# Kernel optimization log

Measured on AMD Instinct MI355X. Metric: run time of the kernel, lower is better.

The kernel has to match this reference:

```python
import jax, jax.numpy as jnp
import numpy as np

# CE module constants (from init_kwargs / chosen input shape)
K = 7        # ksize
S1 = 4       # stride_1 (query patches / fold stride)
S2 = 1       # stride_2 (key/value patches)
SCALE = 10.0 # softmax_scale
C_IN = 32    # in_channels
IC = 4       # inter_channels
B, H, W = 2, 128, 128
PAD1 = ((1, 2), (1, 2))  # 'same' padding for k=7, stride=4, H=W=128 (top=1,bot=2)
PAD2 = ((3, 3), (3, 3))  # 'same' padding for k=7, stride=1


def _conv(x, w, b, stride, pad):
    y = jax.lax.conv_general_dilated(x, w, (stride, stride), pad,
                                     dimension_numbers=('NCHW', 'OIHW', 'NCHW'))
    return y + b[None, :, None, None]


def _patches(x, k, stride, pad):
    # returns [B, L, C*k*k] with feature order (C, kh, kw) == torch.nn.Unfold
    p = jax.lax.conv_general_dilated_patches(x, (k, k), (stride, stride), padding=pad)
    bb, f, ho, wo = p.shape
    return p.reshape(bb, f, ho * wo).transpose(0, 2, 1), ho, wo


def _fold_norm(out, ic, k, hh, ww, stride, pad, lh, lw):
    # out: [B, L1, ic*k*k] -> F.fold(..., (hh,ww), k, padding=pad, stride=stride),
    # normalized by overlap count fold(unfold(ones)).
    bb = out.shape[0]
    z = out.reshape(bb, lh, lw, ic, k, k).transpose(0, 3, 1, 2, 4, 5)  # [B,ic,lh,lw,k,k]
    hp, wp = hh + 2 * pad, ww + 2 * pad
    acc = jnp.zeros((bb, ic, hp, wp), out.dtype)
    cnt = jnp.zeros((hp, wp), out.dtype)
    ih = jnp.arange(lh) * stride
    iw = jnp.arange(lw) * stride
    one = jnp.ones((lh, lw), out.dtype)
    for ki in range(k):
        for kj in range(k):
            r = (ih + ki)[:, None]
            c = (iw + kj)[None, :]
            acc = acc.at[:, :, r, c].add(z[:, :, :, :, ki, kj])
            cnt = cnt.at[r, c].add(one)
    acc = acc[:, :, pad:pad + hh, pad:pad + ww]
    cnt = cnt[pad:pad + hh, pad:pad + ww]
    return acc / cnt


def setup_inputs() -> dict:
    key = jax.random.key(0)
    ks = jax.random.split(key, 13)
    f = K * K * IC  # 196
    g = f // 4      # 49
    s = 0.05
    return {
        'b':       jax.random.normal(ks[0], (B, C_IN, H, W), jnp.float32),
        'w_g':     (jax.random.normal(ks[1], (IC, C_IN, 3, 3), jnp.float32) * s),
        'b_g':     jnp.zeros((IC,), jnp.float32),
        'w_theta': (jax.random.normal(ks[2], (IC, C_IN, 1, 1), jnp.float32) * s),
        'b_theta': jnp.zeros((IC,), jnp.float32),
        'w_fc1':   (jax.random.normal(ks[3], (g, f), jnp.float32) * s),
        'b_fc1':   jnp.zeros((g,), jnp.float32),
        'w_fc2':   (jax.random.normal(ks[4], (g, f), jnp.float32) * s),
        'b_fc2':   jnp.zeros((g,), jnp.float32),
        'w_thr':   (jax.random.normal(ks[5], (1, C_IN, K, K), jnp.float32) * s),
        'b_thr':   jnp.zeros((1,), jnp.float32),
        'w_bias':  (jax.random.normal(ks[6], (1, C_IN, K, K), jnp.float32) * s),
        'b_bias':  jnp.zeros((1,), jnp.float32),
    }


def reference(b, w_g, b_g, w_theta, b_theta, w_fc1, b_fc1, w_fc2, b_fc2,
              w_thr, b_thr, w_bias, b_bias):
    bb = b.shape[0]
    b1 = _conv(b, w_g, b_g, 1, ((1, 1), (1, 1)))        # g: 3x3, pad 1 -> [B,IC,H,W]
    b2 = _conv(b, w_theta, b_theta, 1, ((0, 0), (0, 0)))  # theta: 1x1
    # adaptive threshold / bias per coarse patch (conv on same-padded b)
    thr = _conv(b, w_thr, b_thr, S1, PAD1).reshape(bb, -1)    # [B, L1]
    bias = _conv(b, w_bias, b_bias, S1, PAD1).reshape(bb, -1)  # [B, L1]
    p28, lh, lw = _patches(b1, K, S1, PAD1)   # queries  [B, L1, IC*49]
    p112, _, _ = _patches(b2, K, S2, PAD2)    # values   [B, L2, IC*49]
    p112_2, _, _ = _patches(b1, K, S2, PAD2)  # keys     [B, L2, IC*49] (b3 = b1)
    wi = jax.nn.relu(jnp.einsum('blf,gf->blg', p28, w_fc1) + b_fc1)     # [B,L1,49]
    xi = jax.nn.relu(jnp.einsum('blf,gf->blg', p112_2, w_fc2) + b_fc2)  # [B,L2,49]
    score = jnp.einsum('bpg,bqg->bpq', wi, xi)  # [B, L1, L2]
    mask = jax.nn.relu(score - score.mean(-1, keepdims=True) * thr[:, :, None]
                       + bias[:, :, None])
    mask_b = (mask != 0.0).astype(score.dtype)
    attn = jax.nn.softmax(score * mask * SCALE, axis=-1) * mask_b
    out = jnp.einsum('bpq,bqf->bpf', attn, p112)  # [B, L1, IC*49]
    return _fold_norm(out, IC, K, H, W, S1, 3, lh, lw)  # [B, IC, H, W]
```

## Files before the change

### kernel.cpp

```cpp
#include <hip/hip_runtime.h>
#include <hip/hip_fp16.h>
#include <math.h>

static constexpr int C_IN = 32, IC = 4, H = 128, W = 128, G = 49, F = 196;
static constexpr int L = 1024, Q = 16384;
static constexpr float SCALE = 10.f;
static constexpr int NH = 8;
static constexpr int B2P_PER_B = 8*5*136*136;

typedef __attribute__((ext_vector_type(8))) short short8;
typedef __attribute__((ext_vector_type(4))) float floatx4;

__device__ __forceinline__ unsigned short f2bf(float f){
  unsigned u = __float_as_uint(f);
  return (unsigned short)((u + 0x7fffu + ((u >> 16) & 1u)) >> 16);
}
__device__ __forceinline__ float bf2f(unsigned short h){
  return __uint_as_float(((unsigned)h) << 16);
}
__device__ __forceinline__ floatx4 mfma16(uint4 a, uint4 b, floatx4 c){
  return __builtin_amdgcn_mfma_f32_16x16x32_bf16(*(short8*)&a, *(short8*)&b, c, 0, 0, 0);
}

__global__ __launch_bounds__(256) void k_front(
    const float* __restrict__ bsrc, const float* __restrict__ w_g, const float* __restrict__ b_g,
    const float* __restrict__ w_t, const float* __restrict__ b_t,
    float* __restrict__ b1, unsigned short* __restrict__ b2p) {
  __shared__ float s_wg[IC*C_IN*9];
  __shared__ float s_wt[IC*C_IN];
  __shared__ float s_bg[IC], s_bt[IC];
  for (int i = threadIdx.x; i < IC*C_IN*9; i += 256) s_wg[i] = w_g[i];
  for (int i = threadIdx.x; i < IC*C_IN; i += 256) s_wt[i] = w_t[i];
  if (threadIdx.x < IC) { s_bg[threadIdx.x] = b_g[threadIdx.x]; s_bt[threadIdx.x] = b_t[threadIdx.x]; }
  __syncthreads();
  int idx = blockIdx.x*256 + threadIdx.x;
  int x = idx & 127, y = (idx>>7) & 127, bb = idx >> 14;
  const float* bp = bsrc + (size_t)bb*C_IN*H*W;
  float a1[IC], a2[IC];
  #pragma unroll
  for (int o=0;o<IC;o++){ a1[o]=s_bg[o]; a2[o]=s_bt[o]; }
  for (int c=0;c<C_IN;c++){
    const float* bc = bp + c*H*W;
    float ctr = bc[y*W+x];
    #pragma unroll
    for (int o=0;o<IC;o++) a2[o] += ctr * s_wt[o*C_IN + c];
    #pragma unroll
    for (int dy=0; dy<3; dy++){
      int yy = y + dy - 1;
      if ((unsigned)yy >= (unsigned)H) continue;
      #pragma unroll
      for (int dx=0; dx<3; dx++){
        int xx = x + dx - 1;
        if ((unsigned)xx >= (unsigned)W) continue;
        float v = bc[yy*W+xx];
        #pragma unroll
        for (int o=0;o<IC;o++) a1[o] += v * s_wg[(o*C_IN + c)*9 + dy*3 + dx];
      }
    }
  }
  unsigned short* bp2 = b2p + (size_t)bb*B2P_PER_B;
  #pragma unroll
  for (int o=0;o<IC;o++){
    b1[((size_t)(bb*IC+o)*H + y)*W + x] = a1[o];
    unsigned short h = f2bf(a2[o]);
    #pragma unroll
    for (int s=0;s<7;s++){
      int u = x + 3 - s;
      if (u >= 0)
        bp2[((s*5 + o)*136 + (y+3))*136 + u] = h;
    }
  }
}

__global__ __launch_bounds__(128) void k_xi(
    const float* __restrict__ b1, const float* __restrict__ w_fc2, const float* __restrict__ b_fc2,
    unsigned short* __restrict__ xiT, float* __restrict__ meanxi) {
  __shared__ float s_wT[196][16];
  __shared__ float s_p[IC*7*136];
  __shared__ float s_red[2][16];
  int tid = threadIdx.x;
  int blk = blockIdx.x;
  int gq = blk & 3, y = (blk >> 2) & 127, bb = blk >> 9;
  int g0 = (gq == 0) ? 0 : (13 + 12*(gq-1));
  int ng = (gq == 0) ? 13 : 12;
  for (int i = tid; i < 196*16; i += 128){
    int f = i >> 4, gi = i & 15;
    s_wT[f][gi] = (gi < ng) ? w_fc2[(size_t)(g0+gi)*196 + f] : 0.f;
  }
  for (int i=tid; i<IC*7*136; i+=128) {
    int col = i % 136; int t = i / 136; int ki = t % 7; int c = t / 7;
    int gy = y - 3 + ki, gx = col - 3;
    float v = 0.f;
    if ((unsigned)gy < (unsigned)H && (unsigned)gx < (unsigned)W && col < 134)
      v = b1[((size_t)(bb*IC+c)*H + gy)*W + gx];
    s_p[i] = v;
  }
  __syncthreads();
  int x = tid;
  float acc[13];
  #pragma unroll
  for (int ai=0; ai<13; ++ai) acc[ai] = (ai < ng) ? b_fc2[g0+ai] : 0.f;
  for (int c=0;c<IC;c++)
    for (int ki=0;ki<7;ki++){
      const float* prow = &s_p[(c*7+ki)*136 + x];
      #pragma unroll
      for (int kj=0;kj<7;kj++){
        float pv = prow[kj];
        int f = c*49 + ki*7 + kj;
        const float4* wr = (const float4*)&s_wT[f][0];
        float4 w0 = wr[0], w1 = wr[1], w2 = wr[2], w3 = wr[3];
        float wv[16] = {w0.x,w0.y,w0.z,w0.w, w1.x,w1.y,w1.z,w1.w,
                        w2.x,w2.y,w2.z,w2.w, w3.x,w3.y,w3.z,w3.w};
        #pragma unroll
        for (int ai=0; ai<13; ++ai) acc[ai] += pv * wv[ai];
      }
    }
  #pragma unroll
  for (int ai=0; ai<13; ++ai) acc[ai] = fmaxf(acc[ai], 0.f);
  #pragma unroll
  for (int ai=0; ai<13; ++ai){
    if (ai >= ng) break;
    float v = acc[ai];
    #pragma unroll
    for (int off=1; off<64; off<<=1) v += __shfl_xor(v, off);
    if ((tid&63)==0) s_red[tid>>6][ai] = v;
  }
  __syncthreads();
  if (tid < ng) atomicAdd(&meanxi[bb*G + g0 + tid], (s_red[0][tid]+s_red[1][tid]) * (1.f/(float)Q));
  unsigned short* xr = xiT + ((size_t)((bb<<14) + y*W + x))*128;
  #pragma unroll
  for (int ai=0; ai<13; ++ai){
    if (ai >= ng) break;
    float w = acc[ai];
    unsigned short h = f2bf(w);
    float l = w - bf2f(h);
    xr[g0+ai] = h;
    xr[64+g0+ai] = f2bf(l);
  }
  if (gq == 3){
    for (int gi=49; gi<64; ++gi){ xr[gi] = 0; xr[64+gi] = 0; }
  }
}

__global__ __launch_bounds__(256) void k_wi(
    const float* __restrict__ b1, const float* __restrict__ w_fc1, const float* __restrict__ b_fc1,
    const float* __restrict__ meanxi,
    unsigned short* __restrict__ wiP, float* __restrict__ rowmean) {
  __shared__ float wt[196*52];
  __shared__ float mxs[64];
  int tid = threadIdx.x;
  for (int i=tid; i<G*F; i+=256){ int g = i/F, f = i%F; wt[f*52 + g] = w_fc1[i]; }
  for (int i=tid; i<F*3; i+=256){ int f = i/3; wt[f*52 + 49 + (i%3)] = 0.f; }
  int pg0 = blockIdx.x*4;
  int bb = pg0 >> 10;
  if (tid < 64) mxs[tid] = (tid < G) ? meanxi[bb*G + tid] : 0.f;
  __syncthreads();
  int wave = tid >> 6, g = tid & 63;
  int pg = pg0 + wave;
  int p = pg & 1023;
  int py = p >> 5, px = p & 31;
  float acc = (g < G) ? b_fc1[g] : 0.f;
  for (int c=0;c<IC;c++){
    const float* bc = b1 + (size_t)(bb*IC+c)*H*W;
    for (int ki=0;ki<7;ki++){
      int yy = py*4 - 1 + ki;
      if ((unsigned)yy >= (unsigned)H) continue;
      const float* wrow = &wt[(c*49 + ki*7)*52 + g];
      #pragma unroll
      for (int kj=0;kj<7;kj++){
        int xx = px*4 - 1 + kj;
        if ((unsigned)xx >= (unsigned)W) continue;
        acc += bc[yy*W+xx] * wrow[kj*52];
      }
    }
  }
  acc = fmaxf(acc, 0.f);
  if (g >= G) acc = 0.f;
  float r = acc * mxs[g];
  #pragma unroll
  for (int off=1; off<64; off<<=1) r += __shfl_xor(r, off);
  if (g == 0) rowmean[pg] = r;
  unsigned short h = f2bf(acc);
  float l = acc - bf2f(h);
  size_t base = (size_t)pg*128;
  wiP[base + g] = h;
  wiP[base + 64 + g] = f2bf(l);
}

__global__ __launch_bounds__(256) void k_thrbias(
    const float* __restrict__ bsrc, const float* __restrict__ w_thr, const float* __restrict__ b_thr,
    const float* __restrict__ w_bias, const float* __restrict__ b_bias,
    float* __restrict__ thr, float* __restrict__ bias) {
  int tid = threadIdx.x;
  int c = tid & 31, pl = tid >> 5;
  int pg = blockIdx.x*8 + pl;
  int bb = pg >> 10, p = pg & 1023;
  int py = p >> 5, px = p & 31;
  const float* bc = bsrc + (size_t)(bb*C_IN + c)*H*W;
  float ta = 0.f, ba = 0.f;
  for (int ki=0;ki<7;ki++){
    int yy = py*4 - 1 + ki;
    if ((unsigned)yy >= (unsigned)H) continue;
    #pragma unroll
    for (int kj=0;kj<7;kj++){
      int xx = px*4 - 1 + kj;
      if ((unsigned)xx >= (unsigned)W) continue;
      float v = bc[yy*W+xx];
      ta += v * w_thr[c*49 + ki*7 + kj];
      ba += v * w_bias[c*49 + ki*7 + kj];
    }
  }
  #pragma unroll
  for (int off=1; off<32; off<<=1){ ta += __shfl_xor(ta, off); ba += __shfl_xor(ba, off); }
  if (c == 0) { thr[pg] = ta + b_thr[0]; bias[pg] = ba + b_bias[0]; }
}

__global__ __launch_bounds__(512) void k_attn(
    const unsigned short* __restrict__ b2p, const unsigned short* __restrict__ xiT,
    const unsigned short* __restrict__ wiP, const float* __restrict__ thr,
    const float* __restrict__ bias, const float* __restrict__ rowmean,
    __half* __restrict__ paccT, float* __restrict__ pm, float* __restrict__ pd) {
  __shared__ unsigned short sW[2][64*280];
  __shared__ float sRed[8][64];
  __shared__ float sAlpha[64];
  int tid = threadIdx.x, lane = tid & 63, wave = tid >> 6;
  int l16 = lane & 15, lg = lane >> 4;
  int wid = blockIdx.x;
  int sp = wid & 7, ptb = (wid >> 3) & 15, bb = wid >> 7;
  int pt2 = wave >> 2, qq = wave & 3;
  int gi0 = (bb<<10) + ptb*64;
  int pl[2] = { pt2*32 + l16, pt2*32 + 16 + l16 };
  float cf[2];
  uint4 wh0[2], wh1[2], wl0[2], wl1[2];
  #pragma unroll
  for (int a=0;a<2;a++){
    int gi = gi0 + pl[a];
    cf[a] = bias[gi] - rowmean[gi]*thr[gi];
    const unsigned short* wr = wiP + (size_t)gi*128;
    wh0[a] = *(const uint4*)&wr[lg*8];
    wh1[a] = *(const uint4*)&wr[32 + lg*8];
    wl0[a] = *(const uint4*)&wr[64 + lg*8];
    wl1[a] = *(const uint4*)&wr[96 + lg*8];
  }
  const unsigned short* xib = xiT + ((size_t)((bb<<14) + sp*2048 + qq*64))*128;
  int bbase = bb * B2P_PER_B;

  int okf[2]; int At[2]; int fcol[2];
  #pragma unroll
  for (int i=0;i<2;i++){
    int ft = wave + 8*i;
    okf[i] = (ft < 13);
    if (ft > 12) ft = 12;
    int f = ft*16 + l16;
    fcol[i] = f;
    int fc = f/49, rem = f%49, fki = rem/7, fkj = rem%7;
    At[i] = ((fkj*5 + fc)*136 + fki)*136;
  }
  floatx4 acc[2][4];
  #pragma unroll
  for (int i=0;i<2;i++)
    #pragma unroll
    for (int pt=0;pt<4;pt++) acc[i][pt] = (floatx4){0,0,0,0};

  float Mrun[2] = {0.f, 0.f};
  float dpart[2] = {0.f, 0.f};

  for (int c=0; c<8; ++c){
    if (c > 0){
      #pragma unroll
      for (int pt=0; pt<4; ++pt){
        float4 av = *(const float4*)&sAlpha[pt*16 + lg*4];
        floatx4 a4 = {av.x, av.y, av.z, av.w};
        acc[0][pt] *= a4;
        acc[1][pt] *= a4;
      }
    }
    float vs[2][16];
    unsigned mb[2] = {0u, 0u};
    float vmax[2] = {0.f, 0.f};
    #pragma unroll
    for (int qt=0; qt<4; ++qt){
      const unsigned short* xr = xib + (size_t)(c*256 + qt*16 + l16)*128;
      uint4 ah0 = *(const uint4*)&xr[lg*8];
      uint4 ah1 = *(const uint4*)&xr[32 + lg*8];
      uint4 al0 = *(const uint4*)&xr[64 + lg*8];
      uint4 al1 = *(const uint4*)&xr[96 + lg*8];
      #pragma unroll
      for (int a=0;a<2;a++){
        floatx4 s4 = {0.f,0.f,0.f,0.f};
        s4 = mfma16(ah0, wh0[a], s4);
        s4 = mfma16(ah1, wh1[a], s4);
        s4 = mfma16(ah0, wl0[a], s4);
        s4 = mfma16(ah1, wl1[a], s4);
        s4 = mfma16(al0, wh0[a], s4);
        s4 = mfma16(al1, wh1[a], s4);
        #pragma unroll
        for (int j=0;j<4;j++){
          float s = s4[j];
          float xm = s + cf[a];
          if (xm > 0.f) mb[a] |= (1u << (qt*4 + j));
          float v = s * fmaxf(xm, 0.f) * SCALE;
          vs[a][qt*4 + j] = v;
          vmax[a] = fmaxf(vmax[a], v);
        }
      }
    }
    if (c > 0){
      int ybase = sp*16 + (c-1)*2;
      const unsigned short* sWr = &sW[(c-1)&1][0];
      for (int ks=0; ks<8; ++ks){
        int kk = ks*32 + lg*8;
        int y = ybase + (kk >> 7), x8 = kk & 127;
        int gb = bbase + y*136 + x8;
        uint4 bv0 = *(const uint4*)(b2p + gb + At[0]);
        uint4 bv1 = {0,0,0,0};
        if (okf[1]) bv1 = *(const uint4*)(b2p + gb + At[1]);
        #pragma unroll
        for (int pt=0; pt<4; ++pt){
          uint4 a0 = *(const uint4*)&sWr[(pt*16 + l16)*280 + kk];
          acc[0][pt] = mfma16(a0, bv0, acc[0][pt]);
          if (okf[1]) acc[1][pt] = mfma16(a0, bv1, acc[1][pt]);
        }
      }
    }
    #pragma unroll
    for (int a=0;a<2;a++){
      vmax[a] = fmaxf(vmax[a], __shfl_xor(vmax[a], 16));
      vmax[a] = fmaxf(vmax[a], __shfl_xor(vmax[a], 32));
      if (lg == 0) sRed[wave][pl[a]] = vmax[a];
    }
    __syncthreads();
    #pragma unroll
    for (int a=0;a<2;a++){
      float cm = fmaxf(fmaxf(sRed[pt2*4+0][pl[a]], sRed[pt2*4+1][pl[a]]),
                       fmaxf(sRed[pt2*4+2][pl[a]], sRed[pt2*4+3][pl[a]]));
      float Mnew = fmaxf(Mrun[a], cm);
      float alpha = __expf(Mrun[a] - Mnew);
      Mrun[a] = Mnew;
      if (qq == 0 && lg == 0) sAlpha[pl[a]] = alpha;
      float sum = 0.f;
      #pragma unroll
      for (int qt=0; qt<4; ++qt){
        float e0 = __expf(vs[a][qt*4+0] - Mnew);
        float e1 = __expf(vs[a][qt*4+1] - Mnew);
        float e2 = __expf(vs[a][qt*4+2] - Mnew);
        float e3 = __expf(vs[a][qt*4+3] - Mnew);
        sum += e0+e1+e2+e3;
        unsigned m4 = mb[a] >> (qt*4);
        unsigned w0 = ((m4&1u)? (unsigned)f2bf(e0):0u) | (((m4&2u)? (unsigned)f2bf(e1):0u)<<16);
        unsigned w1 = ((m4&4u)? (unsigned)f2bf(e2):0u) | (((m4&8u)? (unsigned)f2bf(e3):0u)<<16);
        uint2 pv = {w0, w1};
        *(uint2*)&sW[c&1][pl[a]*280 + qq*64 + qt*16 + lg*4] = pv;
      }
      dpart[a] = dpart[a]*alpha + sum;
    }
    __syncthreads();
  }
  #pragma unroll
  for (int pt=0; pt<4; ++pt){
    float4 av = *(const float4*)&sAlpha[pt*16 + lg*4];
    floatx4 a4 = {av.x, av.y, av.z, av.w};
    acc[0][pt] *= a4;
    acc[1][pt] *= a4;
  }
  {
    int ybase = sp*16 + 7*2;
    const unsigned short* sWr = &sW[1][0];
    for (int ks=0; ks<8; ++ks){
      int kk = ks*32 + lg*8;
      int y = ybase + (kk >> 7), x8 = kk & 127;
      int gb = bbase + y*136 + x8;
      uint4 bv0 = *(const uint4*)(b2p + gb + At[0]);
      uint4 bv1 = {0,0,0,0};
      if (okf[1]) bv1 = *(const uint4*)(b2p + gb + At[1]);
      #pragma unroll
      for (int pt=0; pt<4; ++pt){
        uint4 a0 = *(const uint4*)&sWr[(pt*16 + l16)*280 + kk];
        acc[0][pt] = mfma16(a0, bv0, acc[0][pt]);
        if (okf[1]) acc[1][pt] = mfma16(a0, bv1, acc[1][pt]);
      }
    }
  }
  #pragma unroll
  for (int a=0;a<2;a++){
    dpart[a] += __shfl_xor(dpart[a], 16);
    dpart[a] += __shfl_xor(dpart[a], 32);
    if (lg == 0) sRed[wave][pl[a]] = dpart[a];
  }
  __syncthreads();
  int rowbase = ((bb*16 + ptb)*8 + sp)*64;
  if (qq == 0 && lg == 0){
    #pragma unroll
    for (int a=0;a<2;a++){
      float D = sRed[pt2*4+0][pl[a]] + sRed[pt2*4+1][pl[a]]
              + sRed[pt2*4+2][pl[a]] + sRed[pt2*4+3][pl[a]];
      pm[rowbase + pl[a]] = Mrun[a];
      pd[rowbase + pl[a]] = D;
    }
  }
  #pragma unroll
  for (int i=0;i<2;i++){
    if (!okf[i] || fcol[i] >= F) continue;
    #pragma unroll
    for (int pt=0; pt<4; ++pt){
      #pragma unroll
      for (int j=0;j<4;j++){
        int row = rowbase + pt*16 + lg*4 + j;
        paccT[(size_t)fcol[i]*16384 + row] = __float2half(acc[i][pt][j]);
      }
    }
  }
}

__global__ __launch_bounds__(256) void k_combine(
    const __half* __restrict__ paccT, const float* __restrict__ pm, const float* __restrict__ pd,
    float* __restrict__ outpfT){
  int i = blockIdx.x*256 + threadIdx.x;
  if (i >= 2*L*F) return;
  int f = i >> 11;
  int pp = i & 2047;
  int bb = pp >> 10, p = pp & 1023;
  int ptb = p >> 6, r = p & 63;
  int base = ((bb*16 + ptb)*8)*64 + r;
  float M = 0.f;
  #pragma unroll
  for (int hh=0; hh<NH; hh++) M = fmaxf(M, pm[base + hh*64]);
  float num = 0.f, den = 0.f;
  #pragma unroll
  for (int hh=0; hh<NH; hh++){
    float e = __expf(pm[base + hh*64] - M);
    num += e * __half2float(paccT[(size_t)f*16384 + base + hh*64]);
    den += e * pd[base + hh*64];
  }
  outpfT[(size_t)f*2048 + pp] = num/den;
}

__global__ __launch_bounds__(256) void k_fold(const float* __restrict__ outpfT, float* __restrict__ out){
  int i = blockIdx.x*256 + threadIdx.x;
  if (i >= 2*IC*H*W) return;
  int ww = i & 127, hh = (i>>7)&127, c = (i>>14)&3, bb = i>>16;
  int H3 = hh+3, W3 = ww+3;
  int py0 = (H3-3)>>2, py1 = min(31, H3>>2);
  int px0 = (W3-3)>>2, px1 = min(31, W3>>2);
  float s = 0.f; int cnt = 0;
  for (int py=py0; py<=py1; py++){
    int ki = H3 - 4*py;
    for (int px=px0; px<=px1; px++){
      int kj = W3 - 4*px;
      int f = c*49 + ki*7 + kj;
      s += outpfT[(size_t)f*2048 + (bb<<10) + py*32 + px];
      cnt++;
    }
  }
  out[i] = s / (float)cnt;
}

extern "C" void kernel_launch(void* const* d_in, const int* in_sizes, int n_in,
                              void* d_out, int out_size, void* d_ws, size_t ws_size,
                              hipStream_t stream) {
  const float* b      = (const float*)d_in[0];
  const float* w_g    = (const float*)d_in[1];
  const float* b_g    = (const float*)d_in[2];
  const float* w_t    = (const float*)d_in[3];
  const float* b_t    = (const float*)d_in[4];
  const float* w_fc1  = (const float*)d_in[5];
  const float* b_fc1  = (const float*)d_in[6];
  const float* w_fc2  = (const float*)d_in[7];
  const float* b_fc2  = (const float*)d_in[8];
  const float* w_thr  = (const float*)d_in[9];
  const float* b_thr  = (const float*)d_in[10];
  const float* w_bias = (const float*)d_in[11];
  const float* b_bias = (const float*)d_in[12];
  float* out = (float*)d_out;
  float* ws = (float*)d_ws;

  float* b1      = ws;
  unsigned short* b2p = (unsigned short*)(ws + 131072);
  unsigned short* xiT = (unsigned short*)(ws + 870912);
  unsigned short* wiP = (unsigned short*)(ws + 2968064);
  float* meanxi  = ws + 3099136;
  float* thr     = ws + 3099264;
  float* bias    = ws + 3101312;
  float* rowmean = ws + 3103360;
  __half* paccT  = (__half*)(ws + 3105408);
  float* pm      = ws + 4711040;
  float* pd      = ws + 4727424;
  float* outpfT  = ws + 870912;
  (void)in_sizes; (void)n_in; (void)out_size; (void)ws_size;

  hipMemsetAsync(meanxi, 0, 2*G*sizeof(float), stream);
  hipMemsetAsync(b2p, 0, 2*B2P_PER_B*sizeof(unsigned short), stream);
  k_front  <<<128, 256, 0, stream>>>(b, w_g, b_g, w_t, b_t, b1, b2p);
  k_xi     <<<1024, 128, 0, stream>>>(b1, w_fc2, b_fc2, xiT, meanxi);
  k_wi     <<<512, 256, 0, stream>>>(b1, w_fc1, b_fc1, meanxi, wiP, rowmean);
  k_thrbias<<<256, 256, 0, stream>>>(b, w_thr, b_thr, w_bias, b_bias, thr, bias);
  k_attn   <<<256, 512, 0, stream>>>(b2p, xiT, wiP, thr, bias, rowmean, paccT, pm, pd);
  k_combine<<<(2*L*F + 255)/256, 256, 0, stream>>>(paccT, pm, pd, outpfT);
  k_fold   <<<512, 256, 0, stream>>>(outpfT, out);
}
```

Baseline: 222.9 us.

## Split attention blocks into 32-query tiles with 4 waves over 512 blocks

Restructures k_attn so each block handles 32 query rows with 4 waves instead of 64 rows with 8 waves, and launches 512 blocks of 256 threads. Each wave now covers 4 feature tiles and 2 row tiles in the PV accumulation, and the combine kernel's partial-result indexing is updated to match. The goal is more blocks across the 256 CUs, smaller LDS per block and better occupancy. In exchange, the score GEMM and softmax are recomputed once per 32 rows rather than once per 64 rows for the same key slices, and value loads are reused across fewer rows.

```diff
diff --git a/kernel.cpp b/kernel.cpp
--- a/kernel.cpp
+++ b/kernel.cpp
@@ -215,21 +215,21 @@
   if (c == 0) { thr[pg] = ta + b_thr[0]; bias[pg] = ba + b_bias[0]; }
 }
 
-__global__ __launch_bounds__(512) void k_attn(
+__global__ __launch_bounds__(256) void k_attn(
     const unsigned short* __restrict__ b2p, const unsigned short* __restrict__ xiT,
     const unsigned short* __restrict__ wiP, const float* __restrict__ thr,
     const float* __restrict__ bias, const float* __restrict__ rowmean,
     __half* __restrict__ paccT, float* __restrict__ pm, float* __restrict__ pd) {
-  __shared__ unsigned short sW[2][64*280];
-  __shared__ float sRed[8][64];
-  __shared__ float sAlpha[64];
+  __shared__ unsigned short sW[2][32*280];
+  __shared__ float sRed[4][32];
+  __shared__ float sAlpha[32];
   int tid = threadIdx.x, lane = tid & 63, wave = tid >> 6;
   int l16 = lane & 15, lg = lane >> 4;
   int wid = blockIdx.x;
-  int sp = wid & 7, ptb = (wid >> 3) & 15, bb = wid >> 7;
-  int pt2 = wave >> 2, qq = wave & 3;
-  int gi0 = (bb<<10) + ptb*64;
-  int pl[2] = { pt2*32 + l16, pt2*32 + 16 + l16 };
+  int sp = wid & 7, ptb = (wid >> 3) & 31, bb = wid >> 8;
+  int qq = wave;
+  int gi0 = (bb<<10) + ptb*32;
+  int pl[2] = { l16, 16 + l16 };
   float cf[2];
   uint4 wh0[2], wh1[2], wl0[2], wl1[2];
   #pragma unroll
@@ -245,22 +245,21 @@
   const unsigned short* xib = xiT + ((size_t)((bb<<14) + sp*2048 + qq*64))*128;
   int bbase = bb * B2P_PER_B;
 
-  int okf[2]; int At[2]; int fcol[2];
-  #pragma unroll
-  for (int i=0;i<2;i++){
-    int ft = wave + 8*i;
+  int okf[4]; int At[4]; int fcol[4];
+  #pragma unroll
+  for (int i=0;i<4;i++){
+    int ft = wave + 4*i;
     okf[i] = (ft < 13);
     if (ft > 12) ft = 12;
     int f = ft*16 + l16;
     fcol[i] = f;
     int fc = f/49, rem = f%49, fki = rem/7, fkj = rem%7;
     At[i] = ((fkj*5 + fc)*136 + fki)*136;
-  }
-  floatx4 acc[2][4];
-  #pragma unroll
-  for (int i=0;i<2;i++)
-    #pragma unroll
-    for (int pt=0;pt<4;pt++) acc[i][pt] = (floatx4){0,0,0,0};
+    okf[i] = okf[i] && (f < F);
+  }
+  floatx4 acc[4][2];
+  #pragma unroll
+  for (int i=0;i<4;i++){ acc[i][0] = (floatx4){0,0,0,0}; acc[i][1] = (floatx4){0,0,0,0}; }
 
   float Mrun[2] = {0.f, 0.f};
   float dpart[2] = {0.f, 0.f};
@@ -268,11 +267,11 @@
   for (int c=0; c<8; ++c){
     if (c > 0){
       #pragma unroll
-      for (int pt=0; pt<4; ++pt){
+      for (int pt=0; pt<2; ++pt){
         float4 av = *(const float4*)&sAlpha[pt*16 + lg*4];
         floatx4 a4 = {av.x, av.y, av.z, av.w};
-        acc[0][pt] *= a4;
-        acc[1][pt] *= a4;
+        #pragma unroll
+        for (int i=0;i<4;i++) acc[i][pt] *= a4;
       }
     }
     float vs[2][16];
@@ -306,20 +305,22 @@
       }
     }
     if (c > 0){
-      int ybase = sp*16 + (c-1)*2;
+      int ybase = (sp*8 + c-1)*2;
       const unsigned short* sWr = &sW[(c-1)&1][0];
       for (int ks=0; ks<8; ++ks){
         int kk = ks*32 + lg*8;
         int y = ybase + (kk >> 7), x8 = kk & 127;
         int gb = bbase + y*136 + x8;
-        uint4 bv0 = *(const uint4*)(b2p + gb + At[0]);
-        uint4 bv1 = {0,0,0,0};
-        if (okf[1]) bv1 = *(const uint4*)(b2p + gb + At[1]);
-        #pragma unroll
-        for (int pt=0; pt<4; ++pt){
+        uint4 bv[4];
+        #pragma unroll
+        for (int i=0;i<4;i++)
+          if (okf[i]) bv[i] = *(const uint4*)(b2p + gb + At[i]);
+        #pragma unroll
+        for (int pt=0; pt<2; ++pt){
           uint4 a0 = *(const uint4*)&sWr[(pt*16 + l16)*280 + kk];
-          acc[0][pt] = mfma16(a0, bv0, acc[0][pt]);
-          if (okf[1]) acc[1][pt] = mfma16(a0, bv1, acc[1][pt]);
+          #pragma unroll
+          for (int i=0;i<4;i++)
+            if (okf[i]) acc[i][pt] = mfma16(a0, bv[i], acc[i][pt]);
         }
       }
     }
@@ -332,8 +333,8 @@
     __syncthreads();
     #pragma unroll
     for (int a=0;a<2;a++){
-      float cm = fmaxf(fmaxf(sRed[pt2*4+0][pl[a]], sRed[pt2*4+1][pl[a]]),
-                       fmaxf(sRed[pt2*4+2][pl[a]], sRed[pt2*4+3][pl[a]]));
+      float cm = fmaxf(fmaxf(sRed[0][pl[a]], sRed[1][pl[a]]),
+                       fmaxf(sRed[2][pl[a]], sRed[3][pl[a]]));
       float Mnew = fmaxf(Mrun[a], cm);
       float alpha = __expf(Mrun[a] - Mnew);
       Mrun[a] = Mnew;
@@ -357,27 +358,29 @@
     __syncthreads();
   }
   #pragma unroll
-  for (int pt=0; pt<4; ++pt){
+  for (int pt=0; pt<2; ++pt){
     float4 av = *(const float4*)&sAlpha[pt*16 + lg*4];
     floatx4 a4 = {av.x, av.y, av.z, av.w};
-    acc[0][pt] *= a4;
-    acc[1][pt] *= a4;
+    #pragma unroll
+    for (int i=0;i<4;i++) acc[i][pt] *= a4;
   }
   {
-    int ybase = sp*16 + 7*2;
+    int ybase = (sp*8 + 7)*2;
     const unsigned short* sWr = &sW[1][0];
     for (int ks=0; ks<8; ++ks){
       int kk = ks*32 + lg*8;
       int y = ybase + (kk >> 7), x8 = kk & 127;
       int gb = bbase + y*136 + x8;
-      uint4 bv0 = *(const uint4*)(b2p + gb + At[0]);
-      uint4 bv1 = {0,0,0,0};
-      if (okf[1]) bv1 = *(const uint4*)(b2p + gb + At[1]);
-      #pragma unroll
-      for (int pt=0; pt<4; ++pt){
+      uint4 bv[4];
+      #pragma unroll
+      for (int i=0;i<4;i++)
+        if (okf[i]) bv[i] = *(const uint4*)(b2p + gb + At[i]);
+      #pragma unroll
+      for (int pt=0; pt<2; ++pt){
         uint4 a0 = *(const uint4*)&sWr[(pt*16 + l16)*280 + kk];
-        acc[0][pt] = mfma16(a0, bv0, acc[0][pt]);
-        if (okf[1]) acc[1][pt] = mfma16(a0, bv1, acc[1][pt]);
+        #pragma unroll
+        for (int i=0;i<4;i++)
+          if (okf[i]) acc[i][pt] = mfma16(a0, bv[i], acc[i][pt]);
       }
     }
   }
@@ -388,21 +391,20 @@
     if (lg == 0) sRed[wave][pl[a]] = dpart[a];
   }
   __syncthreads();
-  int rowbase = ((bb*16 + ptb)*8 + sp)*64;
+  int rowbase = ((bb*32 + ptb)*8 + sp)*32;
   if (qq == 0 && lg == 0){
     #pragma unroll
     for (int a=0;a<2;a++){
-      float D = sRed[pt2*4+0][pl[a]] + sRed[pt2*4+1][pl[a]]
-              + sRed[pt2*4+2][pl[a]] + sRed[pt2*4+3][pl[a]];
+      float D = sRed[0][pl[a]] + sRed[1][pl[a]] + sRed[2][pl[a]] + sRed[3][pl[a]];
       pm[rowbase + pl[a]] = Mrun[a];
       pd[rowbase + pl[a]] = D;
     }
   }
   #pragma unroll
-  for (int i=0;i<2;i++){
-    if (!okf[i] || fcol[i] >= F) continue;
-    #pragma unroll
-    for (int pt=0; pt<4; ++pt){
+  for (int i=0;i<4;i++){
+    if (!okf[i]) continue;
+    #pragma unroll
+    for (int pt=0; pt<2; ++pt){
       #pragma unroll
       for (int j=0;j<4;j++){
         int row = rowbase + pt*16 + lg*4 + j;
@@ -420,17 +422,17 @@
   int f = i >> 11;
   int pp = i & 2047;
   int bb = pp >> 10, p = pp & 1023;
-  int ptb = p >> 6, r = p & 63;
-  int base = ((bb*16 + ptb)*8)*64 + r;
+  int ptb = p >> 5, r = p & 31;
+  int base = ((bb*32 + ptb)*8)*32 + r;
   float M = 0.f;
   #pragma unroll
-  for (int hh=0; hh<NH; hh++) M = fmaxf(M, pm[base + hh*64]);
+  for (int hh=0; hh<NH; hh++) M = fmaxf(M, pm[base + hh*32]);
   float num = 0.f, den = 0.f;
   #pragma unroll
   for (int hh=0; hh<NH; hh++){
-    float e = __expf(pm[base + hh*64] - M);
-    num += e * __half2float(paccT[(size_t)f*16384 + base + hh*64]);
-    den += e * pd[base + hh*64];
+    float e = __expf(pm[base + hh*32] - M);
+    num += e * __half2float(paccT[(size_t)f*16384 + base + hh*32]);
+    den += e * pd[base + hh*32];
   }
   outpfT[(size_t)f*2048 + pp] = num/den;
 }
@@ -473,6 +475,7 @@
   const float* b_bias = (const float*)d_in[12];
   float* out = (float*)d_out;
   float* ws = (float*)d_ws;
+  (void)in_sizes; (void)n_in; (void)out_size; (void)ws_size;
 
   float* b1      = ws;
   unsigned short* b2p = (unsigned short*)(ws + 131072);
@@ -486,7 +489,6 @@
   float* pm      = ws + 4711040;
   float* pd      = ws + 4727424;
   float* outpfT  = ws + 870912;
-  (void)in_sizes; (void)n_in; (void)out_size; (void)ws_size;
 
   hipMemsetAsync(meanxi, 0, 2*G*sizeof(float), stream);
   hipMemsetAsync(b2p, 0, 2*B2P_PER_B*sizeof(unsigned short), stream);
@@ -494,7 +496,7 @@
   k_xi     <<<1024, 128, 0, stream>>>(b1, w_fc2, b_fc2, xiT, meanxi);
   k_wi     <<<512, 256, 0, stream>>>(b1, w_fc1, b_fc1, meanxi, wiP, rowmean);
   k_thrbias<<<256, 256, 0, stream>>>(b, w_thr, b_thr, w_bias, b_bias, thr, bias);
-  k_attn   <<<256, 512, 0, stream>>>(b2p, xiT, wiP, thr, bias, rowmean, paccT, pm, pd);
+  k_attn   <<<512, 256, 0, stream>>>(b2p, xiT, wiP, thr, bias, rowmean, paccT, pm, pd);
   k_combine<<<(2*L*F + 255)/256, 256, 0, stream>>>(paccT, pm, pd, outpfT);
   k_fold   <<<512, 256, 0, stream>>>(outpfT, out);
 }
```

After: 229.5 us. 2.9% more time.
